# Kernel optimization log

Hardware: AMD Instinct MI355X
Metric: run time of the kernel (lower is better)

## Reference

```python
import jax, jax.numpy as jnp
import numpy as np

HEADS = 16
HIDDEN = 1024
DH = HIDDEN // HEADS
STD = 0.02


def setup_inputs() -> dict:
    key = jax.random.key(0)
    ks = jax.random.split(key, 12)
    B, S = 4, 2048
    inp = {
        'q': jax.random.normal(ks[0], (B, S, HIDDEN), jnp.float32),
        'k': jax.random.normal(ks[1], (B, S, HIDDEN), jnp.float32),
        'v': jax.random.normal(ks[2], (B, S, HIDDEN), jnp.float32),
        'mask': jax.random.randint(ks[3], (B, S), 0, 2, jnp.int32),
        # linear layers: weight [out,in] torch-style, init N(0, 0.02), bias 0
        'wq': STD * jax.random.normal(ks[4], (HIDDEN, HIDDEN), jnp.float32),
        'bq': jnp.zeros((HIDDEN,), jnp.float32),
        'wk': STD * jax.random.normal(ks[5], (HIDDEN, HIDDEN), jnp.float32),
        'bk': jnp.zeros((HIDDEN,), jnp.float32),
        'wv': STD * jax.random.normal(ks[6], (HIDDEN, HIDDEN), jnp.float32),
        'bv': jnp.zeros((HIDDEN,), jnp.float32),
        'wo': STD * jax.random.normal(ks[7], (HIDDEN, HIDDEN), jnp.float32),
        'bo': jnp.zeros((HIDDEN,), jnp.float32),
    }
    return inp


def _split_heads(x):
    B, S, _ = x.shape
    return x.reshape(B, S, HEADS, DH).transpose(0, 2, 1, 3)  # [B,H,S,dh]


def reference(q, k, v, mask, wq, bq, wk, bk, wv, bv, wo, bo):
    B, S, _ = q.shape
    qh = _split_heads(q @ wq.T + bq)
    kh = _split_heads(k @ wk.T + bk)
    vh = _split_heads(v @ wv.T + bv)
    scale = 1.0 / jnp.sqrt(jnp.float32(DH))
    corr = jnp.einsum('bhqd,bhkd->bhqk', qh, kh) * scale  # [B,H,S,S]
    # original masks QUERY rows: mask [B,S] -> [B,1,S,1] broadcast over heads & keys
    row_mask = (mask != 0)[:, None, :, None]
    corr = jnp.where(row_mask, corr, jnp.float32(-1e9))
    prob = jax.nn.softmax(corr, axis=-1)
    # dropout p=0.0 (eval / deterministic reference)
    hidden = jnp.einsum('bhqk,bhkd->bhqd', prob, vh)
    hidden = hidden.transpose(0, 2, 1, 3).reshape(B, S, HIDDEN)
    return hidden @ wo.T + bo
```

## Files before the change

### kernel.cpp

```cpp
#include <hip/hip_runtime.h>

#define BATCH 4
#define SEQ 2048
#define HEADS 16
#define DHEAD 64
#define HID 1024
#define MROWS (BATCH * SEQ)
#define QSCALE 0.1803368801111092f

typedef unsigned short u16;
typedef unsigned int u32;
typedef __attribute__((ext_vector_type(4))) float f32x4;
typedef __attribute__((ext_vector_type(8))) short bf16x8;

#define MFMA16(a, b, c) __builtin_amdgcn_mfma_f32_16x16x32_bf16((a), (b), (c), 0, 0, 0)
#define EXP2F(x) __builtin_amdgcn_exp2f(x)

__device__ __forceinline__ u16 f2bf(float f) {
  union { float f; u32 i; } x; x.f = f;
  u32 r = x.i + 0x7fffu + ((x.i >> 16) & 1u);
  return (u16)(r >> 16);
}

__device__ __forceinline__ void lds16(const u16* g, u16* s) {
  __builtin_amdgcn_global_load_lds(
      (const __attribute__((address_space(1))) void*)g,
      (__attribute__((address_space(3))) void*)s, 16, 0, 0);
}

__device__ __forceinline__ void stage8f(const float* __restrict__ g, u16* s) {
  const float4 a = *(const float4*)g;
  const float4 b = *(const float4*)(g + 4);
  ushort4 lo, hi;
  lo.x = f2bf(a.x); lo.y = f2bf(a.y); lo.z = f2bf(a.z); lo.w = f2bf(a.w);
  hi.x = f2bf(b.x); hi.y = f2bf(b.y); hi.z = f2bf(b.z); hi.w = f2bf(b.w);
  *(ushort4*)s = lo;
  *(ushort4*)(s + 4) = hi;
}

struct CvtArgs {
  const float* src[7];
  u16* dst[7];
};
__global__ __launch_bounds__(256) void cvt7(CvtArgs args, int yoff, int nact) {
  const int y = blockIdx.y + yoff;
  const int i = (blockIdx.x * 256 + threadIdx.x) * 8;
  if (y < 3) {
    if (i < nact) stage8f(args.src[y] + i, args.dst[y] + i);
  } else {
    if (i < 4 * (1 << 20)) {
      const int j = i >> 20, off = i & ((1 << 20) - 1);
      stage8f(args.src[3 + j] + off, args.dst[3 + j] + off);
    }
  }
}

template<bool ADMA, bool BDMA>
__device__ __forceinline__ void gemm_core(
    const void* __restrict__ Av, const void* __restrict__ Wv,
    int tid, int m0, int n0, u16* As, u16* Bs, f32x4 (&acc)[4][4])
{
  const int srow = tid >> 2, cslot = tid & 3;
  const int gc = cslot ^ ((srow >> 1) & 3);
  const int w = tid >> 6, l = tid & 63;
  const int quad = l >> 4, l15 = l & 15;
  const int sw = (l15 >> 1) & 3;
  const int wm = (w & 1) << 6, wn = (w >> 1) << 6;

  for (int k0 = 0; k0 < HID; k0 += 32) {
    if (ADMA) {
      const u16* ag = (const u16*)Av + (size_t)(m0 + srow) * HID + k0 + gc * 8;
      lds16(ag, &As[tid * 8]);
      lds16(ag + (size_t)64 * HID, &As[2048 + tid * 8]);
    } else {
      const float* ag = (const float*)Av + (size_t)(m0 + srow) * HID + k0 + gc * 8;
      stage8f(ag, &As[srow * 32 + cslot * 8]);
      stage8f(ag + (size_t)64 * HID, &As[(64 + srow) * 32 + cslot * 8]);
    }
    if (BDMA) {
      const u16* bg = (const u16*)Wv + (size_t)(n0 + srow) * HID + k0 + gc * 8;
      lds16(bg, &Bs[tid * 8]);
      lds16(bg + (size_t)64 * HID, &Bs[2048 + tid * 8]);
    } else {
      const float* bg = (const float*)Wv + (size_t)(n0 + srow) * HID + k0 + gc * 8;
      stage8f(bg, &Bs[srow * 32 + cslot * 8]);
      stage8f(bg + (size_t)64 * HID, &Bs[(64 + srow) * 32 + cslot * 8]);
    }
    __syncthreads();

    bf16x8 a[4], b[4];
    #pragma unroll
    for (int i = 0; i < 4; ++i)
      a[i] = *(const bf16x8*)&As[(wm + i * 16 + l15) * 32 + (quad ^ sw) * 8];
    #pragma unroll
    for (int j = 0; j < 4; ++j)
      b[j] = *(const bf16x8*)&Bs[(wn + j * 16 + l15) * 32 + (quad ^ sw) * 8];
    #pragma unroll
    for (int i = 0; i < 4; ++i)
      #pragma unroll
      for (int j = 0; j < 4; ++j)
        acc[i][j] = MFMA16(a[i], b[j], acc[i][j]);
    __syncthreads();
  }
}

template<bool ADMA, bool BDMA>
__global__ __launch_bounds__(256) void gemm_qkv(
    const void* __restrict__ xq, const void* __restrict__ xk,
    const void* __restrict__ xv,
    const void* __restrict__ wqv, const void* __restrict__ wkv,
    const void* __restrict__ wvv,
    const float* __restrict__ bq, const float* __restrict__ bk,
    const float* __restrict__ bv, const int* __restrict__ Mask,
    u16* __restrict__ qh, u16* __restrict__ kh, u16* __restrict__ vt)
{
  __shared__ u16 As[128 * 32];
  __shared__ u16 Bs[128 * 32];
  const int z = blockIdx.z;
  const void* A = (z == 0) ? xq : (z == 1) ? xk : xv;
  const void* W = (z == 0) ? wqv : (z == 1) ? wkv : wvv;
  const float* Bias = (z == 0) ? bq : (z == 1) ? bk : bv;

  const int tid = threadIdx.x;
  const int m0 = blockIdx.x << 7, n0 = blockIdx.y << 7;
  f32x4 acc[4][4] = {};
  gemm_core<ADMA, BDMA>(A, W, tid, m0, n0, As, Bs, acc);

  const int w = tid >> 6, l = tid & 63;
  const int quad = l >> 4, l15 = l & 15;
  const int wm = (w & 1) << 6, wn = (w >> 1) << 6;

  if (z <= 1) {
    u16* Out = (z == 0) ? qh : kh;
    #pragma unroll
    for (int i = 0; i < 4; ++i) {
      float fl[4];
      #pragma unroll
      for (int r = 0; r < 4; ++r) {
        const int m = m0 + wm + i * 16 + (quad << 2) + r;
        fl[r] = (z == 0) ? (Mask[m] ? QSCALE : 0.f) : 1.f;
      }
      #pragma unroll
      for (int j = 0; j < 4; ++j) {
        const int n = n0 + wn + j * 16 + l15;
        const float bias = Bias[n];
        const int h = n >> 6, d = n & 63;
        #pragma unroll
        for (int r = 0; r < 4; ++r) {
          const int m = m0 + wm + i * 16 + (quad << 2) + r;
          const int bb = m >> 11, s = m & (SEQ - 1);
          Out[((size_t)(bb * HEADS + h) * SEQ + s) * DHEAD + d] =
              f2bf((acc[i][j][r] + bias) * fl[r]);
        }
      }
    }
  } else {
    const int sblk = (m0 + wm) & (SEQ - 1);
    const int bb = (m0 + wm) >> 11;
    #pragma unroll
    for (int j = 0; j < 4; ++j) {
      const int n = n0 + wn + j * 16 + l15;
      const float bias = Bias[n];
      const int h = n >> 6, d = n & 63;
      u16* base = vt + ((size_t)(bb * HEADS + h) * DHEAD + d) * SEQ + sblk;
      #pragma unroll
      for (int r = 0; r < 4; ++r) {
        ushort4 pk;
        pk.x = f2bf(acc[0][j][r] + bias);
        pk.y = f2bf(acc[1][j][r] + bias);
        pk.z = f2bf(acc[2][j][r] + bias);
        pk.w = f2bf(acc[3][j][r] + bias);
        *(ushort4*)(base + ((quad << 2) + r) * 4) = pk;
      }
    }
  }
}

template<bool BDMA>
__global__ __launch_bounds__(256) void gemm_out(
    const u16* __restrict__ hidden, const void* __restrict__ wov,
    const float* __restrict__ bo, float* __restrict__ Out)
{
  __shared__ u16 As[128 * 32];
  __shared__ u16 Bs[128 * 32];
  const int tid = threadIdx.x;
  const int m0 = blockIdx.x << 7, n0 = blockIdx.y << 7;
  f32x4 acc[4][4] = {};
  gemm_core<true, BDMA>(hidden, wov, tid, m0, n0, As, Bs, acc);

  const int w = tid >> 6, l = tid & 63;
  const int quad = l >> 4, l15 = l & 15;
  const int wm = (w & 1) << 6, wn = (w >> 1) << 6;
  #pragma unroll
  for (int j = 0; j < 4; ++j) {
    const int n = n0 + wn + j * 16 + l15;
    const float bias = bo[n];
    #pragma unroll
    for (int i = 0; i < 4; ++i) {
      const int mb = m0 + wm + i * 16 + (quad << 2);
      #pragma unroll
      for (int r = 0; r < 4; ++r)
        Out[(size_t)(mb + r) * HID + n] = acc[i][j][r] + bias;
    }
  }
}

__global__ __launch_bounds__(256) void attn_mfma(
    const u16* __restrict__ QH, const u16* __restrict__ KH,
    const u16* __restrict__ VT, u16* __restrict__ Hidden)
{
  __shared__ u16 Qs[2][128 * 32];
  __shared__ u16 Ks[2][64 * 32];
  __shared__ u16 Vt[2][64 * 32];
  __shared__ u16 Ps[128 * 72];

  const int tid = threadIdx.x;
  const int w = tid >> 6, l = tid & 63;
  const int quad = l >> 4, l15 = l & 15;
  const int sw = (l15 >> 1) & 3;
  const int srow = tid >> 2, cslot = tid & 3;
  const int gc = cslot ^ ((srow >> 1) & 3);
  const int bh = blockIdx.y, b = bh >> 4, h = bh & 15;
  const int q0 = blockIdx.x << 7;

  const u16* qbase = QH + (size_t)bh * SEQ * DHEAD;
  const u16* kbase = KH + (size_t)bh * SEQ * DHEAD;
  const u16* vbase = VT + (size_t)bh * DHEAD * SEQ;

  #pragma unroll
  for (int hh = 0; hh < 2; ++hh) {
    lds16(qbase + (size_t)(q0 + srow) * DHEAD + hh * 32 + gc * 8, &Qs[hh][tid * 8]);
    lds16(qbase + (size_t)(q0 + 64 + srow) * DHEAD + hh * 32 + gc * 8, &Qs[hh][2048 + tid * 8]);
  }
  __syncthreads();

  bf16x8 aq[2][2];
  #pragma unroll
  for (int hh = 0; hh < 2; ++hh)
    #pragma unroll
    for (int i = 0; i < 2; ++i)
      aq[hh][i] = *(const bf16x8*)&Qs[hh][(w * 32 + i * 16 + l15) * 32 + (quad ^ sw) * 8];

  float lsum[2][4] = {};
  f32x4 o[2][4] = {};

  for (int t0 = 0; t0 < SEQ; t0 += 64) {
    __syncthreads();
    #pragma unroll
    for (int hh = 0; hh < 2; ++hh) {
      lds16(kbase + (size_t)(t0 + srow) * DHEAD + hh * 32 + gc * 8, &Ks[hh][tid * 8]);
      lds16(vbase + (size_t)srow * SEQ + t0 + hh * 32 + gc * 8, &Vt[hh][tid * 8]);
    }
    __syncthreads();

    f32x4 s[2][4] = {};
    #pragma unroll
    for (int hh = 0; hh < 2; ++hh)
      #pragma unroll
      for (int j = 0; j < 4; ++j) {
        const bf16x8 bk = *(const bf16x8*)&Ks[hh][(j * 16 + l15) * 32 + (quad ^ sw) * 8];
        s[0][j] = MFMA16(aq[hh][0], bk, s[0][j]);
        s[1][j] = MFMA16(aq[hh][1], bk, s[1][j]);
      }

    #pragma unroll
    for (int i = 0; i < 2; ++i)
      #pragma unroll
      for (int r = 0; r < 4; ++r) {
        const float p0 = EXP2F(s[i][0][r]);
        const float p1 = EXP2F(s[i][1][r]);
        const float p2 = EXP2F(s[i][2][r]);
        const float p3 = EXP2F(s[i][3][r]);
        lsum[i][r] += (p0 + p1) + (p2 + p3);
        ushort4 pk;
        pk.x = f2bf(p0); pk.y = f2bf(p1); pk.z = f2bf(p2); pk.w = f2bf(p3);
        *(ushort4*)&Ps[(w * 32 + i * 16 + (quad << 2) + r) * 72 + l15 * 4] = pk;
      }

    #pragma unroll
    for (int hh = 0; hh < 2; ++hh) {
      bf16x8 ap[2];
      #pragma unroll
      for (int i = 0; i < 2; ++i)
        ap[i] = *(const bf16x8*)&Ps[(w * 32 + i * 16 + l15) * 72 + hh * 32 + quad * 8];
      #pragma unroll
      for (int j = 0; j < 4; ++j) {
        const bf16x8 vb = *(const bf16x8*)&Vt[hh][(j * 16 + l15) * 32 + (quad ^ sw) * 8];
        o[0][j] = MFMA16(ap[0], vb, o[0][j]);
        o[1][j] = MFMA16(ap[1], vb, o[1][j]);
      }
    }
  }

  float inv[2][4];
  #pragma unroll
  for (int i = 0; i < 2; ++i)
    #pragma unroll
    for (int r = 0; r < 4; ++r) {
      float t = lsum[i][r];
      #pragma unroll
      for (int off = 1; off < 16; off <<= 1)
        t += __shfl_xor(t, off);
      inv[i][r] = 1.f / t;
    }

  #pragma unroll
  for (int i = 0; i < 2; ++i)
    #pragma unroll
    for (int j = 0; j < 4; ++j)
      #pragma unroll
      for (int r = 0; r < 4; ++r) {
        const int qrow = q0 + w * 32 + i * 16 + (quad << 2) + r;
        Hidden[((size_t)(b * SEQ + qrow)) * HID + h * DHEAD + j * 16 + l15] =
            f2bf(o[i][j][r] * inv[i][r]);
      }
}

extern "C" void kernel_launch(void* const* d_in, const int* in_sizes, int n_in,
                              void* d_out, int out_size, void* d_ws, size_t ws_size,
                              hipStream_t stream) {
  const float* q  = (const float*)d_in[0];
  const float* k  = (const float*)d_in[1];
  const float* v  = (const float*)d_in[2];
  const int* mask = (const int*)d_in[3];
  const float* wq = (const float*)d_in[4];
  const float* bq = (const float*)d_in[5];
  const float* wk = (const float*)d_in[6];
  const float* bk = (const float*)d_in[7];
  const float* wv = (const float*)d_in[8];
  const float* bv = (const float*)d_in[9];
  const float* wo = (const float*)d_in[10];
  const float* bo = (const float*)d_in[11];

  const size_t SEG = (size_t)MROWS * HID;
  const size_t WSEG = (size_t)HID * HID;
  const dim3 gq(MROWS / 128, HID / 128, 3);
  const dim3 go(MROWS / 128, HID / 128);
  const dim3 ga(SEQ / 128, BATCH * HEADS);

  const size_t planFULL = (6 * SEG + 4 * WSEG) * sizeof(u16);
  const size_t planMID  = (4 * SEG + 4 * WSEG) * sizeof(u16);

  if (ws_size >= planFULL) {
    u16* qb  = (u16*)d_ws;
    u16* kb  = qb + SEG;
    u16* vb  = kb + SEG;
    u16* qh  = vb + SEG;
    u16* kh  = qh + SEG;
    u16* vt  = kh + SEG;
    u16* wqb = vt + SEG;
    u16* wkb = wqb + WSEG;
    u16* wvb = wkb + WSEG;
    u16* wob = wvb + WSEG;
    u16* hidden = qb;

    CvtArgs ca;
    ca.src[0] = q;  ca.dst[0] = qb;
    ca.src[1] = k;  ca.dst[1] = kb;
    ca.src[2] = v;  ca.dst[2] = vb;
    ca.src[3] = wq; ca.dst[3] = wqb;
    ca.src[4] = wk; ca.dst[4] = wkb;
    ca.src[5] = wv; ca.dst[5] = wvb;
    ca.src[6] = wo; ca.dst[6] = wob;
    cvt7<<<dim3(SEG / 2048, 4), 256, 0, stream>>>(ca, 0, (int)SEG);

    gemm_qkv<true, true><<<gq, 256, 0, stream>>>(qb, kb, vb, wqb, wkb, wvb,
                                                 bq, bk, bv, mask, qh, kh, vt);
    attn_mfma<<<ga, 256, 0, stream>>>(qh, kh, vt, hidden);
    gemm_out<true><<<go, 256, 0, stream>>>(hidden, wob, bo, (float*)d_out);
  } else if (ws_size >= planMID) {
    u16* wqb = (u16*)d_ws;
    u16* wkb = wqb + WSEG;
    u16* wvb = wkb + WSEG;
    u16* wob = wvb + WSEG;
    u16* qh = wob + WSEG;
    u16* kh = qh + SEG;
    u16* vt = kh + SEG;
    u16* hidden = vt + SEG;

    CvtArgs ca;
    ca.src[0] = ca.src[1] = ca.src[2] = q;
    ca.dst[0] = ca.dst[1] = ca.dst[2] = wqb;
    ca.src[3] = wq; ca.dst[3] = wqb;
    ca.src[4] = wk; ca.dst[4] = wkb;
    ca.src[5] = wv; ca.dst[5] = wvb;
    ca.src[6] = wo; ca.dst[6] = wob;
    cvt7<<<dim3(4 * WSEG / 2048, 1), 256, 0, stream>>>(ca, 3, 0);

    gemm_qkv<false, true><<<gq, 256, 0, stream>>>(q, k, v, wqb, wkb, wvb,
                                                  bq, bk, bv, mask, qh, kh, vt);
    attn_mfma<<<ga, 256, 0, stream>>>(qh, kh, vt, hidden);
    gemm_out<true><<<go, 256, 0, stream>>>(hidden, wob, bo, (float*)d_out);
  } else {
    u16* qh = (u16*)d_ws;
    u16* kh = qh + SEG;
    u16* vt = kh + SEG;
    u16* hidden = vt + SEG;

    gemm_qkv<false, false><<<gq, 256, 0, stream>>>(q, k, v, wq, wk, wv,
                                                   bq, bk, bv, mask, qh, kh, vt);
    attn_mfma<<<ga, 256, 0, stream>>>(qh, kh, vt, hidden);
    gemm_out<false><<<go, 256, 0, stream>>>(hidden, wo, bo, (float*)d_out);
  }
}
```

Before: 377.9 us.

## Use 2-wave attention blocks with 64 query rows per wave and shared Q/P LDS

The attention kernel now runs 128 threads (2 waves), each wave owning 64 query rows instead of 32. This doubles MFMA reuse of each K/V fragment loaded from LDS. The Q staging buffer is reused as the swizzled P buffer to cut LDS footprint, and the block index is remapped so consecutive blocks cover different heads. The cost is more accumulator registers per thread (a 4x4 tile for both o and s), which can limit occupancy, and fewer threads to share the K/V loads.

```diff
diff --git a/kernel.cpp b/kernel.cpp
--- a/kernel.cpp
+++ b/kernel.cpp
@@ -205,14 +205,13 @@
   }
 }
 
-__global__ __launch_bounds__(256) void attn_mfma(
+__global__ __launch_bounds__(128, 2) void attn_mfma(
     const u16* __restrict__ QH, const u16* __restrict__ KH,
     const u16* __restrict__ VT, u16* __restrict__ Hidden)
 {
-  __shared__ u16 Qs[2][128 * 32];
+  __shared__ u16 QP[128 * 64];
   __shared__ u16 Ks[2][64 * 32];
   __shared__ u16 Vt[2][64 * 32];
-  __shared__ u16 Ps[128 * 72];
 
   const int tid = threadIdx.x;
   const int w = tid >> 6, l = tid & 63;
@@ -220,51 +219,61 @@
   const int sw = (l15 >> 1) & 3;
   const int srow = tid >> 2, cslot = tid & 3;
   const int gc = cslot ^ ((srow >> 1) & 3);
-  const int bh = blockIdx.y, b = bh >> 4, h = bh & 15;
-  const int q0 = blockIdx.x << 7;
+
+  const int lin = blockIdx.y * 16 + blockIdx.x;
+  const int bh = lin & 63, b = bh >> 4, h = bh & 15;
+  const int q0 = (lin >> 6) << 7;
 
   const u16* qbase = QH + (size_t)bh * SEQ * DHEAD;
   const u16* kbase = KH + (size_t)bh * SEQ * DHEAD;
   const u16* vbase = VT + (size_t)bh * DHEAD * SEQ;
 
   #pragma unroll
-  for (int hh = 0; hh < 2; ++hh) {
-    lds16(qbase + (size_t)(q0 + srow) * DHEAD + hh * 32 + gc * 8, &Qs[hh][tid * 8]);
-    lds16(qbase + (size_t)(q0 + 64 + srow) * DHEAD + hh * 32 + gc * 8, &Qs[hh][2048 + tid * 8]);
-  }
+  for (int hh = 0; hh < 2; ++hh)
+    #pragma unroll
+    for (int part = 0; part < 4; ++part)
+      lds16(qbase + (size_t)(q0 + part * 32 + srow) * DHEAD + hh * 32 + gc * 8,
+            &QP[hh * 4096 + part * 1024 + tid * 8]);
   __syncthreads();
 
-  bf16x8 aq[2][2];
+  bf16x8 aq[2][4];
   #pragma unroll
   for (int hh = 0; hh < 2; ++hh)
     #pragma unroll
-    for (int i = 0; i < 2; ++i)
-      aq[hh][i] = *(const bf16x8*)&Qs[hh][(w * 32 + i * 16 + l15) * 32 + (quad ^ sw) * 8];
-
-  float lsum[2][4] = {};
-  f32x4 o[2][4] = {};
+    for (int i = 0; i < 4; ++i)
+      aq[hh][i] = *(const bf16x8*)
+          &QP[hh * 4096 + (w * 64 + i * 16 + l15) * 32 + (quad ^ sw) * 8];
+
+  float lsum[4][4] = {};
+  f32x4 o[4][4] = {};
 
   for (int t0 = 0; t0 < SEQ; t0 += 64) {
     __syncthreads();
     #pragma unroll
-    for (int hh = 0; hh < 2; ++hh) {
-      lds16(kbase + (size_t)(t0 + srow) * DHEAD + hh * 32 + gc * 8, &Ks[hh][tid * 8]);
-      lds16(vbase + (size_t)srow * SEQ + t0 + hh * 32 + gc * 8, &Vt[hh][tid * 8]);
-    }
+    for (int hh = 0; hh < 2; ++hh)
+      #pragma unroll
+      for (int part = 0; part < 2; ++part) {
+        lds16(kbase + (size_t)(t0 + part * 32 + srow) * DHEAD + hh * 32 + gc * 8,
+              &Ks[hh][part * 1024 + tid * 8]);
+        lds16(vbase + (size_t)(part * 32 + srow) * SEQ + t0 + hh * 32 + gc * 8,
+              &Vt[hh][part * 1024 + tid * 8]);
+      }
     __syncthreads();
 
-    f32x4 s[2][4] = {};
-    #pragma unroll
-    for (int hh = 0; hh < 2; ++hh)
-      #pragma unroll
-      for (int j = 0; j < 4; ++j) {
-        const bf16x8 bk = *(const bf16x8*)&Ks[hh][(j * 16 + l15) * 32 + (quad ^ sw) * 8];
-        s[0][j] = MFMA16(aq[hh][0], bk, s[0][j]);
-        s[1][j] = MFMA16(aq[hh][1], bk, s[1][j]);
-      }
-
-    #pragma unroll
-    for (int i = 0; i < 2; ++i)
+    f32x4 s[4][4] = {};
+    #pragma unroll
+    for (int j = 0; j < 4; ++j)
+      #pragma unroll
+      for (int hh = 0; hh < 2; ++hh) {
+        const bf16x8 bk = *(const bf16x8*)
+            &Ks[hh][(j * 16 + l15) * 32 + (quad ^ sw) * 8];
+        #pragma unroll
+        for (int i = 0; i < 4; ++i)
+          s[i][j] = MFMA16(aq[hh][i], bk, s[i][j]);
+      }
+
+    #pragma unroll
+    for (int i = 0; i < 4; ++i)
       #pragma unroll
       for (int r = 0; r < 4; ++r) {
         const float p0 = EXP2F(s[i][0][r]);
@@ -272,29 +281,36 @@
         const float p2 = EXP2F(s[i][2][r]);
         const float p3 = EXP2F(s[i][3][r]);
         lsum[i][r] += (p0 + p1) + (p2 + p3);
+        const int row = w * 64 + i * 16 + (quad << 2) + r;
+        const int cs = ((l15 >> 1) ^ (row & 7)) * 8 + (l15 & 1) * 4;
         ushort4 pk;
         pk.x = f2bf(p0); pk.y = f2bf(p1); pk.z = f2bf(p2); pk.w = f2bf(p3);
-        *(ushort4*)&Ps[(w * 32 + i * 16 + (quad << 2) + r) * 72 + l15 * 4] = pk;
+        *(ushort4*)&QP[row * 64 + cs] = pk;
       }
 
     #pragma unroll
     for (int hh = 0; hh < 2; ++hh) {
-      bf16x8 ap[2];
-      #pragma unroll
-      for (int i = 0; i < 2; ++i)
-        ap[i] = *(const bf16x8*)&Ps[(w * 32 + i * 16 + l15) * 72 + hh * 32 + quad * 8];
+      bf16x8 ap[4];
+      #pragma unroll
+      for (int i = 0; i < 4; ++i) {
+        const int row = w * 64 + i * 16 + l15;
+        ap[i] = *(const bf16x8*)
+            &QP[row * 64 + (((hh * 4 + quad) ^ (row & 7)) << 3)];
+      }
       #pragma unroll
       for (int j = 0; j < 4; ++j) {
-        const bf16x8 vb = *(const bf16x8*)&Vt[hh][(j * 16 + l15) * 32 + (quad ^ sw) * 8];
-        o[0][j] = MFMA16(ap[0], vb, o[0][j]);
-        o[1][j] = MFMA16(ap[1], vb, o[1][j]);
-      }
-    }
-  }
-
-  float inv[2][4];
+        const bf16x8 vb = *(const bf16x8*)
+            &Vt[hh][(j * 16 + l15) * 32 + (quad ^ sw) * 8];
+        #pragma unroll
+        for (int i = 0; i < 4; ++i)
+          o[i][j] = MFMA16(ap[i], vb, o[i][j]);
+      }
+    }
+  }
+
+  float inv[4][4];
   #pragma unroll
-  for (int i = 0; i < 2; ++i)
+  for (int i = 0; i < 4; ++i)
     #pragma unroll
     for (int r = 0; r < 4; ++r) {
       float t = lsum[i][r];
@@ -305,12 +321,12 @@
     }
 
   #pragma unroll
-  for (int i = 0; i < 2; ++i)
+  for (int i = 0; i < 4; ++i)
     #pragma unroll
     for (int j = 0; j < 4; ++j)
       #pragma unroll
       for (int r = 0; r < 4; ++r) {
-        const int qrow = q0 + w * 32 + i * 16 + (quad << 2) + r;
+        const int qrow = q0 + w * 64 + i * 16 + (quad << 2) + r;
         Hidden[((size_t)(b * SEQ + qrow)) * HID + h * DHEAD + j * 16 + l15] =
             f2bf(o[i][j][r] * inv[i][r]);
       }
@@ -366,7 +382,7 @@
 
     gemm_qkv<true, true><<<gq, 256, 0, stream>>>(qb, kb, vb, wqb, wkb, wvb,
                                                  bq, bk, bv, mask, qh, kh, vt);
-    attn_mfma<<<ga, 256, 0, stream>>>(qh, kh, vt, hidden);
+    attn_mfma<<<ga, 128, 0, stream>>>(qh, kh, vt, hidden);
     gemm_out<true><<<go, 256, 0, stream>>>(hidden, wob, bo, (float*)d_out);
   } else if (ws_size >= planMID) {
     u16* wqb = (u16*)d_ws;
@@ -389,7 +405,7 @@
 
     gemm_qkv<false, true><<<gq, 256, 0, stream>>>(q, k, v, wqb, wkb, wvb,
                                                   bq, bk, bv, mask, qh, kh, vt);
-    attn_mfma<<<ga, 256, 0, stream>>>(qh, kh, vt, hidden);
+    attn_mfma<<<ga, 128, 0, stream>>>(qh, kh, vt, hidden);
     gemm_out<true><<<go, 256, 0, stream>>>(hidden, wob, bo, (float*)d_out);
   } else {
     u16* qh = (u16*)d_ws;
@@ -399,7 +415,7 @@
 
     gemm_qkv<false, false><<<gq, 256, 0, stream>>>(q, k, v, wq, wk, wv,
                                                    bq, bk, bv, mask, qh, kh, vt);
-    attn_mfma<<<ga, 256, 0, stream>>>(qh, kh, vt, hidden);
+    attn_mfma<<<ga, 128, 0, stream>>>(qh, kh, vt, hidden);
     gemm_out<false><<<go, 256, 0, stream>>>(hidden, wo, bo, (float*)d_out);
   }
 }
```

Measured after the change: 358.9 us. 1.05x faster.
